# Performance work log

Hardware: AMD Instinct MI355X
Metric: run time of the kernel (lower is better)

## Reference

```python
import jax, jax.numpy as jnp
import numpy as np

SPLINE_ORDER = 3
GRID_SIZE = 1
# efficient-kan style grid over [-1,1], extended by spline_order on each side; h = 2/grid_size = 2
GRID = jnp.arange(-SPLINE_ORDER, GRID_SIZE + SPLINE_ORDER + 1, dtype=jnp.float32) * 2.0 - 1.0
NB = GRID_SIZE + SPLINE_ORDER  # 4 basis functions per input feature
EPS = 1e-5


def b_splines(x, grid):
    # x: [..., in] -> [..., in, NB] via Cox-de Boor recursion
    xe = x[..., None]
    b = ((xe >= grid[:-1]) & (xe < grid[1:])).astype(x.dtype)
    for p in range(1, SPLINE_ORDER + 1):
        b = ((xe - grid[:-(p + 1)]) / (grid[p:-1] - grid[:-(p + 1)]) * b[..., :-1]
             + (grid[p + 1:] - xe) / (grid[p + 1:] - grid[1:-p]) * b[..., 1:])
    return b


def kan_linear(x, base_w, spline_w):
    # base branch: silu(x) @ W_base^T ; spline branch: B(x) contracted with W_spline [out,in,NB]
    base = jnp.einsum('...i,oi->...o', jax.nn.silu(x), base_w)
    sp = jnp.einsum('...ik,oik->...o', b_splines(x, GRID), spline_w)
    return base + sp


def kan_conv2x2(x, base_w, spline_w):
    # x: [B,C,H,W] -> [B,C_out,H-1,W-1]
    p = jax.lax.conv_general_dilated_patches(x, (2, 2), (1, 1), 'VALID')  # [B, C*4, H', W']
    p = jnp.moveaxis(p, 1, -1)  # [B,H',W',C*4]
    y = kan_linear(p, base_w, spline_w)  # [B,H',W',C_out]
    return jnp.moveaxis(y, -1, 1)


def bn2d(x, g, b):
    m = x.mean((0, 2, 3), keepdims=True)
    v = x.var((0, 2, 3), keepdims=True)
    return (x - m) * jax.lax.rsqrt(v + EPS) * g[None, :, None, None] + b[None, :, None, None]


def bn1d(x, g, b):
    m = x.mean(0, keepdims=True)
    v = x.var(0, keepdims=True)
    return (x - m) * jax.lax.rsqrt(v + EPS) * g[None, :] + b[None, :]


def maxpool2(x):
    B, C, H, W = x.shape
    Hc, Wc = (H // 2) * 2, (W // 2) * 2
    return x[:, :, :Hc, :Wc].reshape(B, C, H // 2, 2, W // 2, 2).max((3, 5))


def setup_inputs() -> dict:
    key = jax.random.key(0)
    ks = jax.random.split(key, 16)
    f32 = jnp.float32
    d = {
        'x': jax.random.normal(ks[0], (1024, 3, 32, 32), f32),
        'base_w1': jax.random.normal(ks[1], (32, 12), f32) * 0.2,
        'spline_w1': jax.random.normal(ks[2], (32, 12, NB), f32) * 0.1,
        'bn1_g': jnp.ones((32,), f32), 'bn1_b': jnp.zeros((32,), f32),
        'base_w2': jax.random.normal(ks[3], (64, 128), f32) * 0.08,
        'spline_w2': jax.random.normal(ks[4], (64, 128, NB), f32) * 0.04,
        'bn2_g': jnp.ones((64,), f32), 'bn2_b': jnp.zeros((64,), f32),
        'fc1_w': jax.random.normal(ks[5], (64, 3136), f32) * 0.02,
        'fc1_b': jnp.zeros((64,), f32),
        'bn3_g': jnp.ones((64,), f32), 'bn3_b': jnp.zeros((64,), f32),
        'fc2_w': jax.random.normal(ks[6], (10, 64), f32) * 0.1,
        'fc2_b': jnp.zeros((10,), f32),
    }
    return d


def reference(x, base_w1, spline_w1, bn1_g, bn1_b, base_w2, spline_w2, bn2_g, bn2_b,
              fc1_w, fc1_b, bn3_g, bn3_b, fc2_w, fc2_b):
    h = kan_conv2x2(x, base_w1, spline_w1)            # [B,32,31,31]
    h = jax.nn.relu(bn2d(h, bn1_g, bn1_b))
    h = maxpool2(h)                                   # [B,32,15,15]
    h = kan_conv2x2(h, base_w2, spline_w2)            # [B,64,14,14]
    h = jax.nn.relu(bn2d(h, bn2_g, bn2_b))
    h = maxpool2(h)                                   # [B,64,7,7]
    h = h.reshape(h.shape[0], -1)                     # [B,3136]
    h = h @ fc1_w.T + fc1_b
    h = jax.nn.relu(bn1d(h, bn3_g, bn3_b))
    # Dropout is identity at inference
    return h @ fc2_w.T + fc2_b                        # [B,10]
```

## Files before the change

kernel.cpp:

```cpp
#include <hip/hip_runtime.h>
#include <math.h>

#define BN_EPS 1e-5f

typedef __attribute__((ext_vector_type(8))) _Float16 f16x8;
typedef __attribute__((ext_vector_type(4))) _Float16 f16x4;
typedef __attribute__((ext_vector_type(2))) __fp16 fp16v2;
typedef __attribute__((ext_vector_type(4))) float f32x4;


__device__ __forceinline__ float siluf(float v) {
    return v * __builtin_amdgcn_rcpf(1.0f + __expf(-v));
}

__device__ __forceinline__ void expand5(float v, float f[5]) {
    f[0] = siluf(v);
    float u = (v + 7.0f) * 0.5f;
#pragma unroll
    for (int i = 0; i < 4; ++i) {
        float a = fabsf(u - (float)(i + 2));
        float p = fmaxf(2.0f - a, 0.0f);
        float q = fmaxf(1.0f - a, 0.0f);
        f[i + 1] = p * p * p - 4.0f * (q * q * q);
    }
}

__device__ __forceinline__ int pkh(float a, float b) {
    union { fp16v2 h2; int i; } u;
    u.h2 = __builtin_amdgcn_cvt_pkrtz(a, b);
    return u.i;
}


__global__ __launch_bounds__(256) void wconv1h_kernel(
        const float* __restrict__ bw, const float* __restrict__ sw,
        _Float16* __restrict__ Wf1) {
    int t = blockIdx.x * 256 + threadIdx.x;
    if (t >= 32 * 64) return;
    int n = t >> 6;
    int k = t & 63;
    int s = k >> 4, j = k & 15;
    float val = 0.f;
    if (j < 15) {
        int f = j / 3, c = j - f * 3;
        int i = c * 4 + s;
        val = (f == 0) ? bw[n * 12 + i]
                       : sw[(n * 12 + i) * 4 + f - 1] * (1.0f / 6.0f);
    }
    Wf1[t] = (_Float16)val;
}


__global__ __launch_bounds__(256, 4) void conv1_kernel(
        const float* __restrict__ x, const _Float16* __restrict__ Wf1,
        _Float16* __restrict__ pooled, float* __restrict__ part) {
    __shared__ _Float16 Eu[1025 * 16];
    __shared__ float Rs[4][64];
    char* EuB = (char*)Eu;

    int t = threadIdx.x;
    int lane = t & 63, wv = t >> 6;
    int quad = lane >> 4, l15 = lane & 15;
    int b = blockIdx.x;

    const _Float16* wb0 = Wf1 + (size_t)l15 * 64 + quad * 8;
    f16x8 bf00 = *(const f16x8*)(wb0);
    f16x8 bf01 = *(const f16x8*)(wb0 + 32);
    f16x8 bf10 = *(const f16x8*)(wb0 + 16 * 64);
    f16x8 bf11 = *(const f16x8*)(wb0 + 16 * 64 + 32);

    float xv[12];
    const float* xb = x + (size_t)b * 3072;
#pragma unroll
    for (int k = 0; k < 12; ++k) xv[k] = xb[t + k * 256];
#pragma unroll
    for (int k = 0; k < 12; ++k) {
        int idx = t + k * 256;
        int c = idx >> 10;
        int pos = idx & 1023;
        float f[5];
        expand5(xv[k], f);
        int rb = pos * 32;
        int key = (pos & 12) << 2;
        *(_Float16*)(EuB + ((rb + c * 2) ^ key))        = (_Float16)f[0];
        *(_Float16*)(EuB + ((rb + (3 + c) * 2) ^ key))  = (_Float16)f[1];
        *(_Float16*)(EuB + ((rb + (6 + c) * 2) ^ key))  = (_Float16)f[2];
        *(_Float16*)(EuB + ((rb + (9 + c) * 2) ^ key))  = (_Float16)f[3];
        *(_Float16*)(EuB + ((rb + (12 + c) * 2) ^ key)) = (_Float16)f[4];
    }
    if (t < 8) *(int*)(EuB + 32768 + t * 4) = 0;
    __syncthreads();

    int dxq = quad >> 1, hb = (quad & 1) * 16;
    int wxv = 8 * wv + (l15 & 7);
    int colb = wxv + dxq;
    int pbase = (colb * 32 + hb) ^ ((colb & 12) << 2);
    bool vx = wxv < 31;
    int pzero = 32768 + hb;
    int wy0 = l15 >> 3;

    float ss0 = 0.f, sq0 = 0.f, ss1 = 0.f, sq1 = 0.f;

    int wy = wy0;
    int p0 = vx ? wy * 1024 + pbase : pzero;
    f16x8 a0 = *(const f16x8*)(EuB + p0);
    f16x8 a1 = *(const f16x8*)(EuB + p0 + (vx ? 1024 : 0));

#pragma unroll 1
    for (int i = 0; i < 16; ++i) {
        f32x4 acc0 = (f32x4){0.f, 0.f, 0.f, 0.f};
        f32x4 acc1 = (f32x4){0.f, 0.f, 0.f, 0.f};
        acc0 = __builtin_amdgcn_mfma_f32_16x16x32_f16(a0, bf00, acc0, 0, 0, 0);
        acc1 = __builtin_amdgcn_mfma_f32_16x16x32_f16(a0, bf10, acc1, 0, 0, 0);
        acc0 = __builtin_amdgcn_mfma_f32_16x16x32_f16(a1, bf01, acc0, 0, 0, 0);
        acc1 = __builtin_amdgcn_mfma_f32_16x16x32_f16(a1, bf11, acc1, 0, 0, 0);
        if (i < 15) {
            int wyn = 2 * (i + 1) + wy0;
            bool vn = vx && (wyn < 31);
            int pn = vn ? wyn * 1024 + pbase : pzero;
            a0 = *(const f16x8*)(EuB + pn);
            a1 = *(const f16x8*)(EuB + pn + (vn ? 1024 : 0));
        }
        float h00 = fmaxf(acc0[0], acc0[1]);
        float h01 = fmaxf(acc0[2], acc0[3]);
        float h10 = fmaxf(acc1[0], acc1[1]);
        float h11 = fmaxf(acc1[2], acc1[3]);
        float g00 = fmaxf(h00, __shfl_down(h00, 32, 64));
        float g01 = fmaxf(h01, __shfl_down(h01, 32, 64));
        float g10 = fmaxf(h10, __shfl_down(h10, 32, 64));
        float g11 = fmaxf(h11, __shfl_down(h11, 32, 64));
        if (lane < 32 && i < 15) {
            int pn0 = 4 * wv + (quad & 1) * 2;
            size_t base = ((size_t)b * 225 + i * 15) * 32;
            if (pn0 < 15) {
                pooled[base + pn0 * 32 + l15]      = (_Float16)g00;
                pooled[base + pn0 * 32 + 16 + l15] = (_Float16)g10;
            }
            if (pn0 < 14) {
                pooled[base + (pn0 + 1) * 32 + l15]      = (_Float16)g01;
                pooled[base + (pn0 + 1) * 32 + 16 + l15] = (_Float16)g11;
            }
        }
        ss0 += acc0[0] + acc0[1] + acc0[2] + acc0[3];
        sq0 += acc0[0] * acc0[0] + acc0[1] * acc0[1]
             + acc0[2] * acc0[2] + acc0[3] * acc0[3];
        ss1 += acc1[0] + acc1[1] + acc1[2] + acc1[3];
        sq1 += acc1[0] * acc1[0] + acc1[1] * acc1[1]
             + acc1[2] * acc1[2] + acc1[3] * acc1[3];
    }

    ss0 += __shfl_down(ss0, 32, 64); ss0 += __shfl_down(ss0, 16, 64);
    sq0 += __shfl_down(sq0, 32, 64); sq0 += __shfl_down(sq0, 16, 64);
    ss1 += __shfl_down(ss1, 32, 64); ss1 += __shfl_down(ss1, 16, 64);
    sq1 += __shfl_down(sq1, 32, 64); sq1 += __shfl_down(sq1, 16, 64);
    if (lane < 16) {
        Rs[wv][2 * l15]          = ss0;
        Rs[wv][2 * l15 + 1]      = sq0;
        Rs[wv][32 + 2 * l15]     = ss1;
        Rs[wv][32 + 2 * l15 + 1] = sq1;
    }
    __syncthreads();
    if (t < 64)
        part[(size_t)b * 64 + t] = Rs[0][t] + Rs[1][t] + Rs[2][t] + Rs[3][t];
}


__global__ __launch_bounds__(256) void wconv16_kernel(
        const float* __restrict__ bw, const float* __restrict__ sw,
        _Float16* __restrict__ Wf) {
    int t = blockIdx.x * 256 + threadIdx.x;
    if (t >= 64 * 640) return;
    int n = t / 640;
    int k = t - n * 640;
    int s = k / 160;
    int r = k - s * 160;
    int f = r >> 5;
    int c = r & 31;
    float val = (f == 0) ? bw[n * 128 + c * 4 + s]
                         : sw[n * 512 + c * 16 + s * 4 + (f - 1)] * (1.0f / 6.0f);
    Wf[t] = (_Float16)val;
}


#define EU_LDW 168

__device__ __forceinline__ void c2_loadb(const _Float16* __restrict__ Wb,
                                         int g, f16x8 bf[5]) {
#pragma unroll
    for (int ks = 0; ks < 5; ++ks)
        bf[ks] = *(const f16x8*)(Wb + g * 160 + ks * 32);
}

__device__ __forceinline__ void c2_mfma(const _Float16* Eu,
                                        const int abase[4][4], int g,
                                        int quad, const f16x8 bf[5],
                                        f32x4 acc[4]) {
#pragma unroll
    for (int ks = 0; ks < 5; ++ks) {
        int jo = ks * 32 + quad * 8;
#pragma unroll
        for (int mt = 0; mt < 4; ++mt) {
            f16x8 a = *(const f16x8*)&Eu[abase[mt][g] + jo];
            acc[mt] = __builtin_amdgcn_mfma_f32_16x16x32_f16(a, bf[ks], acc[mt], 0, 0, 0);
        }
    }
}

__global__ __launch_bounds__(256, 7) void conv2_kernel(
        const _Float16* __restrict__ pooled, const float* __restrict__ stats1,
        const float* __restrict__ g1v, const float* __restrict__ b1v,
        const _Float16* __restrict__ Wf, _Float16* __restrict__ Pt,
        float* __restrict__ part) {
    __shared__ _Float16 Eu[65 * EU_LDW];

    int t = threadIdx.x;
    int lane = t & 63, wv = t >> 6;
    int quad = lane >> 4, l15 = lane & 15;

    int blk = blockIdx.x;
    int b = blk >> 2;
    int py0 = ((blk >> 1) & 1) * 7;
    int px0 = (blk & 1) * 7;

    const _Float16* Wb = Wf + (size_t)(wv * 16 + l15) * 640 + quad * 8;
    f16x8 bfA[5], bfB[5];
    c2_loadb(Wb, 0, bfA);

    {
        int c2 = t & 15, c0 = c2 * 2;
        int xx = (t >> 4) & 7;
        int yh = t >> 7;
        const float invN1 = 1.0f / (1024.0f * 961.0f);
        float m0 = stats1[2 * c0] * invN1;
        float v0 = stats1[2 * c0 + 1] * invN1 - m0 * m0;
        float sc0 = rsqrtf(v0 + BN_EPS) * g1v[c0];
        float sh0 = b1v[c0] - m0 * sc0;
        float m1 = stats1[2 * c0 + 2] * invN1;
        float v1 = stats1[2 * c0 + 3] * invN1 - m1 * m1;
        float sc1 = rsqrtf(v1 + BN_EPS) * g1v[c0 + 1];
        float sh1 = b1v[c0 + 1] - m1 * sc1;
        const _Float16* pbase0 =
            pooled + ((size_t)b * 225 + py0 * 15 + px0) * 32 + c0;
#pragma unroll
        for (int yi = 0; yi < 4; ++yi) {
            int yr = yh * 4 + yi;
            fp16v2 v2 = *(const fp16v2*)(pbase0 + yr * 480 + xx * 32);
            float va = fmaxf((float)v2.x * sc0 + sh0, 0.f);
            float vb = fmaxf((float)v2.y * sc1 + sh1, 0.f);
            float fa[5], fb5[5];
            expand5(va, fa);
            expand5(vb, fb5);
            int* eb = (int*)&Eu[(yr * 8 + xx) * EU_LDW + c0];
            eb[0]  = pkh(fa[0], fb5[0]);
            eb[16] = pkh(fa[1], fb5[1]);
            eb[32] = pkh(fa[2], fb5[2]);
            eb[48] = pkh(fa[3], fb5[3]);
            eb[64] = pkh(fa[4], fb5[4]);
        }
    }
    if (t < 84) *(int*)((char*)&Eu[64 * EU_LDW] + t * 4) = 0;

    int abase[4][4];
#pragma unroll
    for (int mt = 0; mt < 4; ++mt) {
        int m = mt * 16 + l15;
        if (m < 49) {
            int pr = m / 7, pc = m - pr * 7;
#pragma unroll
            for (int s = 0; s < 4; ++s)
                abase[mt][s] = ((pr + (s >> 1)) * 8 + pc + (s & 1)) * EU_LDW;
        } else {
#pragma unroll
            for (int s = 0; s < 4; ++s) abase[mt][s] = 64 * EU_LDW;
        }
    }
    __syncthreads();

    f32x4 acc[4];
#pragma unroll
    for (int mt = 0; mt < 4; ++mt) acc[mt] = (f32x4){0.f, 0.f, 0.f, 0.f};

    c2_loadb(Wb, 1, bfB);
    c2_mfma(Eu, abase, 0, quad, bfA, acc);
    c2_loadb(Wb, 2, bfA);
    c2_mfma(Eu, abase, 1, quad, bfB, acc);
    c2_loadb(Wb, 3, bfB);
    c2_mfma(Eu, abase, 2, quad, bfA, acc);
    c2_mfma(Eu, abase, 3, quad, bfB, acc);

    int o = wv * 16 + l15;
#pragma unroll
    for (int mt = 0; mt < 4; ++mt) {
#pragma unroll
        for (int reg = 0; reg < 4; ++reg) {
            int m = mt * 16 + quad * 4 + reg;
            if (m < 49) {
                int pr = m / 7, pc = m - pr * 7;
                int patch = (b * 14 + py0 + pr) * 14 + px0 + pc;
                Pt[(size_t)patch * 64 + o] = (_Float16)acc[mt][reg];
            }
        }
    }
    float s = 0.f, s2 = 0.f;
#pragma unroll
    for (int mt = 0; mt < 4; ++mt)
#pragma unroll
        for (int reg = 0; reg < 4; ++reg) {
            float a = acc[mt][reg];
            s += a;
            s2 += a * a;
        }
    s  += __shfl_down(s, 16, 64);  s  += __shfl_down(s, 32, 64);
    s2 += __shfl_down(s2, 16, 64); s2 += __shfl_down(s2, 32, 64);
    if (lane < 16) {
        part[(size_t)blk * 128 + 2 * o]     = s;
        part[(size_t)blk * 128 + 2 * o + 1] = s2;
    }
}


__global__ __launch_bounds__(256) void redstats_kernel(
        const float* __restrict__ part, float* __restrict__ stats,
        int nblk, int stride) {
    int p = blockIdx.x;
    float s = 0.f;
    for (int j = threadIdx.x; j < nblk; j += 256)
        s += part[(size_t)j * stride + p];
#pragma unroll
    for (int off = 32; off > 0; off >>= 1) s += __shfl_down(s, off, 64);
    __shared__ float ls[4];
    if ((threadIdx.x & 63) == 0) ls[threadIdx.x >> 6] = s;
    __syncthreads();
    if (threadIdx.x == 0) stats[p] = ls[0] + ls[1] + ls[2] + ls[3];
}


__global__ __launch_bounds__(256) void bnpool2_kernel(
        const _Float16* __restrict__ Pt, const float* __restrict__ stats,
        const float* __restrict__ g, const float* __restrict__ bb,
        _Float16* __restrict__ out) {
    int t = blockIdx.x * 256 + threadIdx.x;
    if (t >= 1024 * 49 * 16) return;
    int c4 = (t & 15) * 4;
    int q2 = (t >> 4) % 49;
    int b  = t / (49 * 16);
    float sc[4], sh[4];
#pragma unroll
    for (int j = 0; j < 4; ++j) {
        int c = c4 + j;
        float mean = stats[2 * c] * (1.0f / 200704.0f);
        float var  = stats[2 * c + 1] * (1.0f / 200704.0f) - mean * mean;
        sc[j] = rsqrtf(var + BN_EPS) * g[c];
        sh[j] = bb[c] - mean * sc[j];
    }
    int py2 = q2 / 7, px2 = q2 - py2 * 7;
    int q = (py2 * 2) * 14 + px2 * 2;
    const _Float16* p = Pt + ((size_t)b * 196 + q) * 64 + c4;
    f16x4 r0 = *(const f16x4*)(p);
    f16x4 r1 = *(const f16x4*)(p + 64);
    f16x4 r2 = *(const f16x4*)(p + 14 * 64);
    f16x4 r3 = *(const f16x4*)(p + 15 * 64);
    f16x4 res;
#pragma unroll
    for (int j = 0; j < 4; ++j) {
        float v0 = fmaxf((float)r0[j] * sc[j] + sh[j], 0.f);
        float v1 = fmaxf((float)r1[j] * sc[j] + sh[j], 0.f);
        float v2 = fmaxf((float)r2[j] * sc[j] + sh[j], 0.f);
        float v3 = fmaxf((float)r3[j] * sc[j] + sh[j], 0.f);
        res[j] = (_Float16)fmaxf(fmaxf(v0, v1), fmaxf(v2, v3));
    }
    *(f16x4*)(out + (size_t)b * 3136 + q2 * 64 + c4) = res;
}


__global__ __launch_bounds__(256) void transpose_kernel(
        const float* __restrict__ w, unsigned int* __restrict__ wTh2) {
    int t = blockIdx.x * 256 + threadIdx.x;
    if (t >= 64 * 1568) return;
    int o = t & 63;
    int j2 = t >> 6;
    int jc = (j2 * 2) & 63;
    int q2 = (j2 * 2) >> 6;
    wTh2[t] = (unsigned int)pkh(w[(size_t)o * 3136 + jc * 49 + q2],
                                w[(size_t)o * 3136 + (jc + 1) * 49 + q2]);
}


__global__ __launch_bounds__(256) void fc1_kernel(
        const _Float16* __restrict__ xin, const unsigned int* __restrict__ wTh2,
        const float* __restrict__ bias, float* __restrict__ z) {
    __shared__ unsigned int xsu[4 * 1568];
    __shared__ float red[4][4][64];
    int b0 = blockIdx.x * 4;
    const unsigned int* xg = (const unsigned int*)xin + (size_t)b0 * 1568;
    for (int j = threadIdx.x; j < 4 * 1568; j += 256) xsu[j] = xg[j];
    __syncthreads();
    int o = threadIdx.x & 63, q = threadIdx.x >> 6;
    float s0 = 0.f, s1 = 0.f, s2 = 0.f, s3 = 0.f;
    const unsigned int* wp = wTh2 + (size_t)q * 392 * 64 + o;
    int jb = q * 392;
    for (int i = 0; i < 392; ++i) {
        union { unsigned int u; fp16v2 h; } uw, u0, u1, u2, u3;
        uw.u = wp[i * 64];
        u0.u = xsu[jb + i];
        u1.u = xsu[1568 + jb + i];
        u2.u = xsu[2 * 1568 + jb + i];
        u3.u = xsu[3 * 1568 + jb + i];
        s0 = __builtin_amdgcn_fdot2(u0.h, uw.h, s0, false);
        s1 = __builtin_amdgcn_fdot2(u1.h, uw.h, s1, false);
        s2 = __builtin_amdgcn_fdot2(u2.h, uw.h, s2, false);
        s3 = __builtin_amdgcn_fdot2(u3.h, uw.h, s3, false);
    }
    red[0][q][o] = s0; red[1][q][o] = s1; red[2][q][o] = s2; red[3][q][o] = s3;
    __syncthreads();
    int bb = threadIdx.x >> 6;
    float tot = red[bb][0][o] + red[bb][1][o] + red[bb][2][o] + red[bb][3][o] + bias[o];
    z[((size_t)(b0 + bb)) * 64 + o] = tot;
}


__global__ __launch_bounds__(256) void colstats_kernel(
        const float* __restrict__ z, const float* __restrict__ g,
        const float* __restrict__ bb, float* __restrict__ scsh) {
    int c = blockIdx.x;
    float s = 0.f, s2 = 0.f;
    for (int b = threadIdx.x; b < 1024; b += 256) {
        float v = z[(size_t)b * 64 + c];
        s += v; s2 += v * v;
    }
#pragma unroll
    for (int off = 32; off > 0; off >>= 1) {
        s  += __shfl_down(s, off, 64);
        s2 += __shfl_down(s2, off, 64);
    }
    __shared__ float ls[8];
    int w = threadIdx.x >> 6;
    if ((threadIdx.x & 63) == 0) { ls[w * 2] = s; ls[w * 2 + 1] = s2; }
    __syncthreads();
    if (threadIdx.x == 0) {
        float st = ls[0] + ls[2] + ls[4] + ls[6];
        float st2 = ls[1] + ls[3] + ls[5] + ls[7];
        float mean = st * (1.0f / 1024.0f);
        float var  = st2 * (1.0f / 1024.0f) - mean * mean;
        float sc = rsqrtf(var + BN_EPS) * g[c];
        scsh[2 * c]     = sc;
        scsh[2 * c + 1] = bb[c] - mean * sc;
    }
}


__global__ __launch_bounds__(256) void final_kernel(
        const float* __restrict__ z, const float* __restrict__ scsh,
        const float* __restrict__ w2, const float* __restrict__ b2,
        float* __restrict__ out) {
    int t = blockIdx.x * 256 + threadIdx.x;
    if (t >= 10240) return;
    int o = t % 10, b = t / 10;
    float acc = b2[o];
#pragma unroll 8
    for (int c = 0; c < 64; ++c) {
        float a = fmaxf(z[(size_t)b * 64 + c] * scsh[2 * c] + scsh[2 * c + 1], 0.f);
        acc += a * w2[o * 64 + c];
    }
    out[t] = acc;
}


extern "C" void kernel_launch(void* const* d_in, const int* in_sizes, int n_in,
                              void* d_out, int out_size, void* d_ws, size_t ws_size,
                              hipStream_t stream) {
    const float* x   = (const float*)d_in[0];
    const float* bw1 = (const float*)d_in[1];
    const float* sw1 = (const float*)d_in[2];
    const float* g1  = (const float*)d_in[3];
    const float* b1  = (const float*)d_in[4];
    const float* bw2 = (const float*)d_in[5];
    const float* sw2 = (const float*)d_in[6];
    const float* g2  = (const float*)d_in[7];
    const float* b2v = (const float*)d_in[8];
    const float* fw1 = (const float*)d_in[9];
    const float* fb1 = (const float*)d_in[10];
    const float* g3  = (const float*)d_in[11];
    const float* b3  = (const float*)d_in[12];
    const float* fw2 = (const float*)d_in[13];
    const float* fb2 = (const float*)d_in[14];
    float* out = (float*)d_out;

    char* ws = (char*)d_ws;
    float* part1     = (float*)(ws);
    _Float16* Pt     = (_Float16*)(ws);
    float* part2     = (float*)(ws + 51380224);
    _Float16* Wf     = (_Float16*)(ws + 100000000);
    _Float16* Wf1    = (_Float16*)(ws + 100131072);
    _Float16* pooled = (_Float16*)(ws + 125960192);
    float* z         = (float*)(ws + 155451392);
    unsigned int* wTh2 = (unsigned int*)(ws + 155713536);
    float* stats1    = (float*)(ws + 156516352);
    float* stats2    = (float*)(ws + 156516608);
    float* stats3    = (float*)(ws + 156517120);

    transpose_kernel<<<392, 256, 0, stream>>>(fw1, wTh2);
    wconv16_kernel<<<160, 256, 0, stream>>>(bw2, sw2, Wf);
    wconv1h_kernel<<<8, 256, 0, stream>>>(bw1, sw1, Wf1);

    conv1_kernel<<<1024, 256, 0, stream>>>(x, Wf1, pooled, part1);
    redstats_kernel<<<64, 256, 0, stream>>>(part1, stats1, 1024, 64);

    conv2_kernel<<<4096, 256, 0, stream>>>(pooled, stats1, g1, b1,
                                           Wf, Pt, part2);
    redstats_kernel<<<128, 256, 0, stream>>>(part2, stats2, 4096, 128);

    _Float16* pooled2 = pooled;
    bnpool2_kernel<<<(1024 * 49 * 16 + 255) / 256, 256, 0, stream>>>(
        Pt, stats2, g2, b2v, pooled2);

    fc1_kernel<<<256, 256, 0, stream>>>(pooled2, wTh2, fb1, z);
    colstats_kernel<<<64, 256, 0, stream>>>(z, g3, b3, stats3);
    final_kernel<<<(10240 + 255) / 256, 256, 0, stream>>>(z, stats3, fw2, fb2, out);
}
```

Before: 196.8 us.

## Merge weight-prep kernels, retile conv2 waves 2x2, halve fc1 batch per block

Three weight-preparation kernels are merged into one launch that dispatches on block index, cutting launch overhead. conv2 changes its wave tiling from four waves each covering all 64 rows for 16 output channels to a 2x2 grid of waves, each covering 32 rows by 32 channels. Weights now load per group inline and BN partial sums are reduced through shared memory, with occupancy lowered from 7 to 6 blocks. fc1 processes 2 batch rows per block with twice as many blocks, adding parallelism at the cost of reading the fc1 weight matrix twice as often.

```diff
diff --git a/kernel.cpp b/kernel.cpp
--- a/kernel.cpp
+++ b/kernel.cpp
@@ -32,22 +32,48 @@
 }
 
 
-__global__ __launch_bounds__(256) void wconv1h_kernel(
-        const float* __restrict__ bw, const float* __restrict__ sw,
+__global__ __launch_bounds__(256) void prep_kernel(
+        const float* __restrict__ fw1, unsigned int* __restrict__ wTh2,
+        const float* __restrict__ bw2, const float* __restrict__ sw2,
+        _Float16* __restrict__ Wf,
+        const float* __restrict__ bw1, const float* __restrict__ sw1,
         _Float16* __restrict__ Wf1) {
-    int t = blockIdx.x * 256 + threadIdx.x;
-    if (t >= 32 * 64) return;
-    int n = t >> 6;
-    int k = t & 63;
-    int s = k >> 4, j = k & 15;
-    float val = 0.f;
-    if (j < 15) {
-        int f = j / 3, c = j - f * 3;
-        int i = c * 4 + s;
-        val = (f == 0) ? bw[n * 12 + i]
-                       : sw[(n * 12 + i) * 4 + f - 1] * (1.0f / 6.0f);
-    }
-    Wf1[t] = (_Float16)val;
+    int blk = blockIdx.x;
+    if (blk < 392) {
+        int t = blk * 256 + threadIdx.x;
+        int o = t & 63;
+        int j2 = t >> 6;
+        int jc = (j2 * 2) & 63;
+        int q2 = (j2 * 2) >> 6;
+        wTh2[t] = (unsigned int)pkh(fw1[(size_t)o * 3136 + jc * 49 + q2],
+                                    fw1[(size_t)o * 3136 + (jc + 1) * 49 + q2]);
+    } else if (blk < 552) {
+        int t = (blk - 392) * 256 + threadIdx.x;
+        if (t >= 64 * 640) return;
+        int n = t / 640;
+        int k = t - n * 640;
+        int s = k / 160;
+        int r = k - s * 160;
+        int f = r >> 5;
+        int c = r & 31;
+        float val = (f == 0) ? bw2[n * 128 + c * 4 + s]
+                             : sw2[n * 512 + c * 16 + s * 4 + (f - 1)] * (1.0f / 6.0f);
+        Wf[t] = (_Float16)val;
+    } else {
+        int t = (blk - 552) * 256 + threadIdx.x;
+        if (t >= 32 * 64) return;
+        int n = t >> 6;
+        int k = t & 63;
+        int s = k >> 4, j = k & 15;
+        float val = 0.f;
+        if (j < 15) {
+            int f = j / 3, c = j - f * 3;
+            int i = c * 4 + s;
+            val = (f == 0) ? bw1[n * 12 + i]
+                           : sw1[(n * 12 + i) * 4 + f - 1] * (1.0f / 6.0f);
+        }
+        Wf1[t] = (_Float16)val;
+    }
 }
 
 
@@ -101,8 +127,7 @@
 
     float ss0 = 0.f, sq0 = 0.f, ss1 = 0.f, sq1 = 0.f;
 
-    int wy = wy0;
-    int p0 = vx ? wy * 1024 + pbase : pzero;
+    int p0 = vx ? wy0 * 1024 + pbase : pzero;
     f16x8 a0 = *(const f16x8*)(EuB + p0);
     f16x8 a1 = *(const f16x8*)(EuB + p0 + (vx ? 1024 : 0));
 
@@ -165,66 +190,28 @@
 }
 
 
-__global__ __launch_bounds__(256) void wconv16_kernel(
-        const float* __restrict__ bw, const float* __restrict__ sw,
-        _Float16* __restrict__ Wf) {
-    int t = blockIdx.x * 256 + threadIdx.x;
-    if (t >= 64 * 640) return;
-    int n = t / 640;
-    int k = t - n * 640;
-    int s = k / 160;
-    int r = k - s * 160;
-    int f = r >> 5;
-    int c = r & 31;
-    float val = (f == 0) ? bw[n * 128 + c * 4 + s]
-                         : sw[n * 512 + c * 16 + s * 4 + (f - 1)] * (1.0f / 6.0f);
-    Wf[t] = (_Float16)val;
-}
-
-
 #define EU_LDW 168
 
-__device__ __forceinline__ void c2_loadb(const _Float16* __restrict__ Wb,
-                                         int g, f16x8 bf[5]) {
-#pragma unroll
-    for (int ks = 0; ks < 5; ++ks)
-        bf[ks] = *(const f16x8*)(Wb + g * 160 + ks * 32);
-}
-
-__device__ __forceinline__ void c2_mfma(const _Float16* Eu,
-                                        const int abase[4][4], int g,
-                                        int quad, const f16x8 bf[5],
-                                        f32x4 acc[4]) {
-#pragma unroll
-    for (int ks = 0; ks < 5; ++ks) {
-        int jo = ks * 32 + quad * 8;
-#pragma unroll
-        for (int mt = 0; mt < 4; ++mt) {
-            f16x8 a = *(const f16x8*)&Eu[abase[mt][g] + jo];
-            acc[mt] = __builtin_amdgcn_mfma_f32_16x16x32_f16(a, bf[ks], acc[mt], 0, 0, 0);
-        }
-    }
-}
-
-__global__ __launch_bounds__(256, 7) void conv2_kernel(
+__global__ __launch_bounds__(256, 6) void conv2_kernel(
         const _Float16* __restrict__ pooled, const float* __restrict__ stats1,
         const float* __restrict__ g1v, const float* __restrict__ b1v,
         const _Float16* __restrict__ Wf, _Float16* __restrict__ Pt,
         float* __restrict__ part) {
     __shared__ _Float16 Eu[65 * EU_LDW];
+    __shared__ float Rs[4][64];
 
     int t = threadIdx.x;
     int lane = t & 63, wv = t >> 6;
     int quad = lane >> 4, l15 = lane & 15;
+    int mw = wv >> 1, nw = wv & 1;
 
     int blk = blockIdx.x;
     int b = blk >> 2;
     int py0 = ((blk >> 1) & 1) * 7;
     int px0 = (blk & 1) * 7;
 
-    const _Float16* Wb = Wf + (size_t)(wv * 16 + l15) * 640 + quad * 8;
-    f16x8 bfA[5], bfB[5];
-    c2_loadb(Wb, 0, bfA);
+    const _Float16* Wb0 = Wf + (size_t)(nw * 32 + l15) * 640 + quad * 8;
+    const _Float16* Wb1 = Wb0 + 16 * 640;
 
     {
         int c2 = t & 15, c0 = c2 * 2;
@@ -260,10 +247,10 @@
     }
     if (t < 84) *(int*)((char*)&Eu[64 * EU_LDW] + t * 4) = 0;
 
-    int abase[4][4];
-#pragma unroll
-    for (int mt = 0; mt < 4; ++mt) {
-        int m = mt * 16 + l15;
+    int abase[2][4];
+#pragma unroll
+    for (int mt = 0; mt < 2; ++mt) {
+        int m = mw * 32 + mt * 16 + l15;
         if (m < 49) {
             int pr = m / 7, pc = m - pr * 7;
 #pragma unroll
@@ -276,45 +263,70 @@
     }
     __syncthreads();
 
-    f32x4 acc[4];
-#pragma unroll
-    for (int mt = 0; mt < 4; ++mt) acc[mt] = (f32x4){0.f, 0.f, 0.f, 0.f};
-
-    c2_loadb(Wb, 1, bfB);
-    c2_mfma(Eu, abase, 0, quad, bfA, acc);
-    c2_loadb(Wb, 2, bfA);
-    c2_mfma(Eu, abase, 1, quad, bfB, acc);
-    c2_loadb(Wb, 3, bfB);
-    c2_mfma(Eu, abase, 2, quad, bfA, acc);
-    c2_mfma(Eu, abase, 3, quad, bfB, acc);
-
-    int o = wv * 16 + l15;
-#pragma unroll
-    for (int mt = 0; mt < 4; ++mt) {
+    f32x4 a00 = (f32x4){0.f, 0.f, 0.f, 0.f};
+    f32x4 a01 = (f32x4){0.f, 0.f, 0.f, 0.f};
+    f32x4 a10 = (f32x4){0.f, 0.f, 0.f, 0.f};
+    f32x4 a11 = (f32x4){0.f, 0.f, 0.f, 0.f};
+
+#pragma unroll
+    for (int g = 0; g < 4; ++g) {
+        f16x8 bf0[5], bf1[5];
+#pragma unroll
+        for (int ks = 0; ks < 5; ++ks) {
+            bf0[ks] = *(const f16x8*)(Wb0 + g * 160 + ks * 32);
+            bf1[ks] = *(const f16x8*)(Wb1 + g * 160 + ks * 32);
+        }
+#pragma unroll
+        for (int ks = 0; ks < 5; ++ks) {
+            int jo = ks * 32 + quad * 8;
+            f16x8 aA = *(const f16x8*)&Eu[abase[0][g] + jo];
+            a00 = __builtin_amdgcn_mfma_f32_16x16x32_f16(aA, bf0[ks], a00, 0, 0, 0);
+            a01 = __builtin_amdgcn_mfma_f32_16x16x32_f16(aA, bf1[ks], a01, 0, 0, 0);
+            f16x8 aB = *(const f16x8*)&Eu[abase[1][g] + jo];
+            a10 = __builtin_amdgcn_mfma_f32_16x16x32_f16(aB, bf0[ks], a10, 0, 0, 0);
+            a11 = __builtin_amdgcn_mfma_f32_16x16x32_f16(aB, bf1[ks], a11, 0, 0, 0);
+        }
+    }
+
+#pragma unroll
+    for (int mt = 0; mt < 2; ++mt) {
 #pragma unroll
         for (int reg = 0; reg < 4; ++reg) {
-            int m = mt * 16 + quad * 4 + reg;
+            int m = mw * 32 + mt * 16 + quad * 4 + reg;
             if (m < 49) {
                 int pr = m / 7, pc = m - pr * 7;
                 int patch = (b * 14 + py0 + pr) * 14 + px0 + pc;
-                Pt[(size_t)patch * 64 + o] = (_Float16)acc[mt][reg];
+                float v0 = (mt == 0) ? a00[reg] : a10[reg];
+                float v1 = (mt == 0) ? a01[reg] : a11[reg];
+                Pt[(size_t)patch * 64 + nw * 32 + l15]      = (_Float16)v0;
+                Pt[(size_t)patch * 64 + nw * 32 + 16 + l15] = (_Float16)v1;
             }
         }
     }
-    float s = 0.f, s2 = 0.f;
-#pragma unroll
-    for (int mt = 0; mt < 4; ++mt)
-#pragma unroll
-        for (int reg = 0; reg < 4; ++reg) {
-            float a = acc[mt][reg];
-            s += a;
-            s2 += a * a;
-        }
-    s  += __shfl_down(s, 16, 64);  s  += __shfl_down(s, 32, 64);
-    s2 += __shfl_down(s2, 16, 64); s2 += __shfl_down(s2, 32, 64);
+    float s0 = 0.f, q0 = 0.f, s1 = 0.f, q1 = 0.f;
+#pragma unroll
+    for (int reg = 0; reg < 4; ++reg) {
+        s0 += a00[reg] + a10[reg];
+        q0 += a00[reg] * a00[reg] + a10[reg] * a10[reg];
+        s1 += a01[reg] + a11[reg];
+        q1 += a01[reg] * a01[reg] + a11[reg] * a11[reg];
+    }
+    s0 += __shfl_down(s0, 16, 64); s0 += __shfl_down(s0, 32, 64);
+    q0 += __shfl_down(q0, 16, 64); q0 += __shfl_down(q0, 32, 64);
+    s1 += __shfl_down(s1, 16, 64); s1 += __shfl_down(s1, 32, 64);
+    q1 += __shfl_down(q1, 16, 64); q1 += __shfl_down(q1, 32, 64);
     if (lane < 16) {
-        part[(size_t)blk * 128 + 2 * o]     = s;
-        part[(size_t)blk * 128 + 2 * o + 1] = s2;
+        Rs[wv][2 * l15]          = s0;
+        Rs[wv][2 * l15 + 1]      = q0;
+        Rs[wv][32 + 2 * l15]     = s1;
+        Rs[wv][32 + 2 * l15 + 1] = q1;
+    }
+    __syncthreads();
+    if (t < 128) {
+        int o = t >> 1;
+        int nwv = o >> 5;
+        int lidx = (o & 31) * 2 + (t & 1);
+        part[(size_t)blk * 128 + t] = Rs[nwv][lidx] + Rs[nwv + 2][lidx];
     }
 }
 
@@ -373,49 +385,36 @@
 }
 
 
-__global__ __launch_bounds__(256) void transpose_kernel(
-        const float* __restrict__ w, unsigned int* __restrict__ wTh2) {
-    int t = blockIdx.x * 256 + threadIdx.x;
-    if (t >= 64 * 1568) return;
-    int o = t & 63;
-    int j2 = t >> 6;
-    int jc = (j2 * 2) & 63;
-    int q2 = (j2 * 2) >> 6;
-    wTh2[t] = (unsigned int)pkh(w[(size_t)o * 3136 + jc * 49 + q2],
-                                w[(size_t)o * 3136 + (jc + 1) * 49 + q2]);
-}
-
-
 __global__ __launch_bounds__(256) void fc1_kernel(
         const _Float16* __restrict__ xin, const unsigned int* __restrict__ wTh2,
         const float* __restrict__ bias, float* __restrict__ z) {
-    __shared__ unsigned int xsu[4 * 1568];
-    __shared__ float red[4][4][64];
-    int b0 = blockIdx.x * 4;
+    __shared__ unsigned int xsu[2 * 1568];
+    __shared__ float red[2][4][64];
+    int b0 = blockIdx.x * 2;
     const unsigned int* xg = (const unsigned int*)xin + (size_t)b0 * 1568;
-    for (int j = threadIdx.x; j < 4 * 1568; j += 256) xsu[j] = xg[j];
+    for (int j = threadIdx.x; j < 2 * 1568; j += 256) xsu[j] = xg[j];
     __syncthreads();
     int o = threadIdx.x & 63, q = threadIdx.x >> 6;
-    float s0 = 0.f, s1 = 0.f, s2 = 0.f, s3 = 0.f;
+    float s0 = 0.f, s1 = 0.f;
     const unsigned int* wp = wTh2 + (size_t)q * 392 * 64 + o;
     int jb = q * 392;
     for (int i = 0; i < 392; ++i) {
-        union { unsigned int u; fp16v2 h; } uw, u0, u1, u2, u3;
+        union { unsigned int u; fp16v2 h; } uw, u0, u1;
         uw.u = wp[i * 64];
         u0.u = xsu[jb + i];
         u1.u = xsu[1568 + jb + i];
-        u2.u = xsu[2 * 1568 + jb + i];
-        u3.u = xsu[3 * 1568 + jb + i];
         s0 = __builtin_amdgcn_fdot2(u0.h, uw.h, s0, false);
         s1 = __builtin_amdgcn_fdot2(u1.h, uw.h, s1, false);
-        s2 = __builtin_amdgcn_fdot2(u2.h, uw.h, s2, false);
-        s3 = __builtin_amdgcn_fdot2(u3.h, uw.h, s3, false);
-    }
-    red[0][q][o] = s0; red[1][q][o] = s1; red[2][q][o] = s2; red[3][q][o] = s3;
-    __syncthreads();
-    int bb = threadIdx.x >> 6;
-    float tot = red[bb][0][o] + red[bb][1][o] + red[bb][2][o] + red[bb][3][o] + bias[o];
-    z[((size_t)(b0 + bb)) * 64 + o] = tot;
+    }
+    red[0][q][o] = s0; red[1][q][o] = s1;
+    __syncthreads();
+    if (threadIdx.x < 128) {
+        int bb = threadIdx.x >> 6;
+        int oo = threadIdx.x & 63;
+        float tot = red[bb][0][oo] + red[bb][1][oo] + red[bb][2][oo]
+                  + red[bb][3][oo] + bias[oo];
+        z[((size_t)(b0 + bb)) * 64 + oo] = tot;
+    }
 }
 
 
@@ -499,9 +498,7 @@
     float* stats2    = (float*)(ws + 156516608);
     float* stats3    = (float*)(ws + 156517120);
 
-    transpose_kernel<<<392, 256, 0, stream>>>(fw1, wTh2);
-    wconv16_kernel<<<160, 256, 0, stream>>>(bw2, sw2, Wf);
-    wconv1h_kernel<<<8, 256, 0, stream>>>(bw1, sw1, Wf1);
+    prep_kernel<<<560, 256, 0, stream>>>(fw1, wTh2, bw2, sw2, Wf, bw1, sw1, Wf1);
 
     conv1_kernel<<<1024, 256, 0, stream>>>(x, Wf1, pooled, part1);
     redstats_kernel<<<64, 256, 0, stream>>>(part1, stats1, 1024, 64);
@@ -514,7 +511,7 @@
     bnpool2_kernel<<<(1024 * 49 * 16 + 255) / 256, 256, 0, stream>>>(
         Pt, stats2, g2, b2v, pooled2);
 
-    fc1_kernel<<<256, 256, 0, stream>>>(pooled2, wTh2, fb1, z);
+    fc1_kernel<<<512, 256, 0, stream>>>(pooled2, wTh2, fb1, z);
     colstats_kernel<<<64, 256, 0, stream>>>(z, g3, b3, stats3);
     final_kernel<<<(10240 + 255) / 256, 256, 0, stream>>>(z, stats3, fw2, fb2, out);
 }
```

New measurement: 227.5 us. 1.16x slower.

## Merge weight-prep kernels, re-pad conv2 LDS layout, and halve fc1 batch per block

Applied to the files above, without the earlier changes.

Fuses the three weight preparation kernels into one launch to cut launch overhead. Changes the conv2 LDS row stride from 168 to 200 halfs with a 40-half per-feature sub-stride, presumably to reduce bank conflicts on the MFMA A-operand loads. That costs more LDS per block, so the occupancy hint drops from 7 to 6. It also halves fc1's batch rows per block to double the grid size, trading weight reuse for more parallelism.

```diff
diff --git a/kernel.cpp b/kernel.cpp
--- a/kernel.cpp
+++ b/kernel.cpp
@@ -32,22 +32,48 @@
 }
 
 
-__global__ __launch_bounds__(256) void wconv1h_kernel(
-        const float* __restrict__ bw, const float* __restrict__ sw,
+__global__ __launch_bounds__(256) void prep_kernel(
+        const float* __restrict__ fw1, unsigned int* __restrict__ wTh2,
+        const float* __restrict__ bw2, const float* __restrict__ sw2,
+        _Float16* __restrict__ Wf,
+        const float* __restrict__ bw1, const float* __restrict__ sw1,
         _Float16* __restrict__ Wf1) {
-    int t = blockIdx.x * 256 + threadIdx.x;
-    if (t >= 32 * 64) return;
-    int n = t >> 6;
-    int k = t & 63;
-    int s = k >> 4, j = k & 15;
-    float val = 0.f;
-    if (j < 15) {
-        int f = j / 3, c = j - f * 3;
-        int i = c * 4 + s;
-        val = (f == 0) ? bw[n * 12 + i]
-                       : sw[(n * 12 + i) * 4 + f - 1] * (1.0f / 6.0f);
-    }
-    Wf1[t] = (_Float16)val;
+    int blk = blockIdx.x;
+    if (blk < 392) {
+        int t = blk * 256 + threadIdx.x;
+        int o = t & 63;
+        int j2 = t >> 6;
+        int jc = (j2 * 2) & 63;
+        int q2 = (j2 * 2) >> 6;
+        wTh2[t] = (unsigned int)pkh(fw1[(size_t)o * 3136 + jc * 49 + q2],
+                                    fw1[(size_t)o * 3136 + (jc + 1) * 49 + q2]);
+    } else if (blk < 552) {
+        int t = (blk - 392) * 256 + threadIdx.x;
+        if (t >= 64 * 640) return;
+        int n = t / 640;
+        int k = t - n * 640;
+        int s = k / 160;
+        int r = k - s * 160;
+        int f = r >> 5;
+        int c = r & 31;
+        float val = (f == 0) ? bw2[n * 128 + c * 4 + s]
+                             : sw2[n * 512 + c * 16 + s * 4 + (f - 1)] * (1.0f / 6.0f);
+        Wf[t] = (_Float16)val;
+    } else {
+        int t = (blk - 552) * 256 + threadIdx.x;
+        if (t >= 32 * 64) return;
+        int n = t >> 6;
+        int k = t & 63;
+        int s = k >> 4, j = k & 15;
+        float val = 0.f;
+        if (j < 15) {
+            int f = j / 3, c = j - f * 3;
+            int i = c * 4 + s;
+            val = (f == 0) ? bw1[n * 12 + i]
+                           : sw1[(n * 12 + i) * 4 + f - 1] * (1.0f / 6.0f);
+        }
+        Wf1[t] = (_Float16)val;
+    }
 }
 
 
@@ -101,8 +127,7 @@
 
     float ss0 = 0.f, sq0 = 0.f, ss1 = 0.f, sq1 = 0.f;
 
-    int wy = wy0;
-    int p0 = vx ? wy * 1024 + pbase : pzero;
+    int p0 = vx ? wy0 * 1024 + pbase : pzero;
     f16x8 a0 = *(const f16x8*)(EuB + p0);
     f16x8 a1 = *(const f16x8*)(EuB + p0 + (vx ? 1024 : 0));
 
@@ -165,24 +190,7 @@
 }
 
 
-__global__ __launch_bounds__(256) void wconv16_kernel(
-        const float* __restrict__ bw, const float* __restrict__ sw,
-        _Float16* __restrict__ Wf) {
-    int t = blockIdx.x * 256 + threadIdx.x;
-    if (t >= 64 * 640) return;
-    int n = t / 640;
-    int k = t - n * 640;
-    int s = k / 160;
-    int r = k - s * 160;
-    int f = r >> 5;
-    int c = r & 31;
-    float val = (f == 0) ? bw[n * 128 + c * 4 + s]
-                         : sw[n * 512 + c * 16 + s * 4 + (f - 1)] * (1.0f / 6.0f);
-    Wf[t] = (_Float16)val;
-}
-
-
-#define EU_LDW 168
+#define EU_PS 200
 
 __device__ __forceinline__ void c2_loadb(const _Float16* __restrict__ Wb,
                                          int g, f16x8 bf[5]) {
@@ -197,7 +205,7 @@
                                         f32x4 acc[4]) {
 #pragma unroll
     for (int ks = 0; ks < 5; ++ks) {
-        int jo = ks * 32 + quad * 8;
+        int jo = ks * 40 + quad * 8;
 #pragma unroll
         for (int mt = 0; mt < 4; ++mt) {
             f16x8 a = *(const f16x8*)&Eu[abase[mt][g] + jo];
@@ -206,12 +214,12 @@
     }
 }
 
-__global__ __launch_bounds__(256, 7) void conv2_kernel(
+__global__ __launch_bounds__(256, 6) void conv2_kernel(
         const _Float16* __restrict__ pooled, const float* __restrict__ stats1,
         const float* __restrict__ g1v, const float* __restrict__ b1v,
         const _Float16* __restrict__ Wf, _Float16* __restrict__ Pt,
         float* __restrict__ part) {
-    __shared__ _Float16 Eu[65 * EU_LDW];
+    __shared__ _Float16 Eu[65 * EU_PS];
 
     int t = threadIdx.x;
     int lane = t & 63, wv = t >> 6;
@@ -250,15 +258,15 @@
             float fa[5], fb5[5];
             expand5(va, fa);
             expand5(vb, fb5);
-            int* eb = (int*)&Eu[(yr * 8 + xx) * EU_LDW + c0];
+            int* eb = (int*)&Eu[(yr * 8 + xx) * EU_PS] + c2;
             eb[0]  = pkh(fa[0], fb5[0]);
-            eb[16] = pkh(fa[1], fb5[1]);
-            eb[32] = pkh(fa[2], fb5[2]);
-            eb[48] = pkh(fa[3], fb5[3]);
-            eb[64] = pkh(fa[4], fb5[4]);
-        }
-    }
-    if (t < 84) *(int*)((char*)&Eu[64 * EU_LDW] + t * 4) = 0;
+            eb[20] = pkh(fa[1], fb5[1]);
+            eb[40] = pkh(fa[2], fb5[2]);
+            eb[60] = pkh(fa[3], fb5[3]);
+            eb[80] = pkh(fa[4], fb5[4]);
+        }
+    }
+    if (t < 100) ((int*)&Eu[64 * EU_PS])[t] = 0;
 
     int abase[4][4];
 #pragma unroll
@@ -268,10 +276,10 @@
             int pr = m / 7, pc = m - pr * 7;
 #pragma unroll
             for (int s = 0; s < 4; ++s)
-                abase[mt][s] = ((pr + (s >> 1)) * 8 + pc + (s & 1)) * EU_LDW;
+                abase[mt][s] = ((pr + (s >> 1)) * 8 + pc + (s & 1)) * EU_PS;
         } else {
 #pragma unroll
-            for (int s = 0; s < 4; ++s) abase[mt][s] = 64 * EU_LDW;
+            for (int s = 0; s < 4; ++s) abase[mt][s] = 64 * EU_PS;
         }
     }
     __syncthreads();
@@ -373,49 +381,36 @@
 }
 
 
-__global__ __launch_bounds__(256) void transpose_kernel(
-        const float* __restrict__ w, unsigned int* __restrict__ wTh2) {
-    int t = blockIdx.x * 256 + threadIdx.x;
-    if (t >= 64 * 1568) return;
-    int o = t & 63;
-    int j2 = t >> 6;
-    int jc = (j2 * 2) & 63;
-    int q2 = (j2 * 2) >> 6;
-    wTh2[t] = (unsigned int)pkh(w[(size_t)o * 3136 + jc * 49 + q2],
-                                w[(size_t)o * 3136 + (jc + 1) * 49 + q2]);
-}
-
-
 __global__ __launch_bounds__(256) void fc1_kernel(
         const _Float16* __restrict__ xin, const unsigned int* __restrict__ wTh2,
         const float* __restrict__ bias, float* __restrict__ z) {
-    __shared__ unsigned int xsu[4 * 1568];
-    __shared__ float red[4][4][64];
-    int b0 = blockIdx.x * 4;
+    __shared__ unsigned int xsu[2 * 1568];
+    __shared__ float red[2][4][64];
+    int b0 = blockIdx.x * 2;
     const unsigned int* xg = (const unsigned int*)xin + (size_t)b0 * 1568;
-    for (int j = threadIdx.x; j < 4 * 1568; j += 256) xsu[j] = xg[j];
+    for (int j = threadIdx.x; j < 2 * 1568; j += 256) xsu[j] = xg[j];
     __syncthreads();
     int o = threadIdx.x & 63, q = threadIdx.x >> 6;
-    float s0 = 0.f, s1 = 0.f, s2 = 0.f, s3 = 0.f;
+    float s0 = 0.f, s1 = 0.f;
     const unsigned int* wp = wTh2 + (size_t)q * 392 * 64 + o;
     int jb = q * 392;
     for (int i = 0; i < 392; ++i) {
-        union { unsigned int u; fp16v2 h; } uw, u0, u1, u2, u3;
+        union { unsigned int u; fp16v2 h; } uw, u0, u1;
         uw.u = wp[i * 64];
         u0.u = xsu[jb + i];
         u1.u = xsu[1568 + jb + i];
-        u2.u = xsu[2 * 1568 + jb + i];
-        u3.u = xsu[3 * 1568 + jb + i];
         s0 = __builtin_amdgcn_fdot2(u0.h, uw.h, s0, false);
         s1 = __builtin_amdgcn_fdot2(u1.h, uw.h, s1, false);
-        s2 = __builtin_amdgcn_fdot2(u2.h, uw.h, s2, false);
-        s3 = __builtin_amdgcn_fdot2(u3.h, uw.h, s3, false);
-    }
-    red[0][q][o] = s0; red[1][q][o] = s1; red[2][q][o] = s2; red[3][q][o] = s3;
-    __syncthreads();
-    int bb = threadIdx.x >> 6;
-    float tot = red[bb][0][o] + red[bb][1][o] + red[bb][2][o] + red[bb][3][o] + bias[o];
-    z[((size_t)(b0 + bb)) * 64 + o] = tot;
+    }
+    red[0][q][o] = s0; red[1][q][o] = s1;
+    __syncthreads();
+    if (threadIdx.x < 128) {
+        int bb = threadIdx.x >> 6;
+        int oo = threadIdx.x & 63;
+        float tot = red[bb][0][oo] + red[bb][1][oo] + red[bb][2][oo]
+                  + red[bb][3][oo] + bias[oo];
+        z[((size_t)(b0 + bb)) * 64 + oo] = tot;
+    }
 }
 
 
@@ -499,9 +494,7 @@
     float* stats2    = (float*)(ws + 156516608);
     float* stats3    = (float*)(ws + 156517120);
 
-    transpose_kernel<<<392, 256, 0, stream>>>(fw1, wTh2);
-    wconv16_kernel<<<160, 256, 0, stream>>>(bw2, sw2, Wf);
-    wconv1h_kernel<<<8, 256, 0, stream>>>(bw1, sw1, Wf1);
+    prep_kernel<<<560, 256, 0, stream>>>(fw1, wTh2, bw2, sw2, Wf, bw1, sw1, Wf1);
 
     conv1_kernel<<<1024, 256, 0, stream>>>(x, Wf1, pooled, part1);
     redstats_kernel<<<64, 256, 0, stream>>>(part1, stats1, 1024, 64);
@@ -514,7 +507,7 @@
     bnpool2_kernel<<<(1024 * 49 * 16 + 255) / 256, 256, 0, stream>>>(
         Pt, stats2, g2, b2v, pooled2);
 
-    fc1_kernel<<<256, 256, 0, stream>>>(pooled2, wTh2, fb1, z);
+    fc1_kernel<<<512, 256, 0, stream>>>(pooled2, wTh2, fb1, z);
     colstats_kernel<<<64, 256, 0, stream>>>(z, g3, b3, stats3);
     final_kernel<<<(10240 + 255) / 256, 256, 0, stream>>>(z, stats3, fw2, fb2, out);
 }
```

New measurement: 190.2 us. 3.4% less time.
